# Kernel tuning notes

Hardware: AMD Instinct MI355X
Metric: run time of the kernel (lower is better)

## Reference

```python
import jax, jax.numpy as jnp
import numpy as np

B, L, S, E = 16, 2048, 2048, 512

def setup_inputs() -> dict:
    key = jax.random.key(0)
    k1, k2, k3 = jax.random.split(key, 3)
    queries = jax.random.normal(k1, (B, L, E), dtype=jnp.float32)
    keys = jax.random.normal(k2, (B, S, E), dtype=jnp.float32)
    values = jax.random.normal(k3, (B, S, E), dtype=jnp.float32)
    # default causal mask: True above the diagonal (positions to mask out)
    attn_mask = jnp.triu(jnp.ones((L, S), dtype=bool), k=1)
    return {"queries": queries, "keys": keys, "values": values, "attn_mask": attn_mask}

def reference(queries, keys, values, attn_mask):
    # queries [B,L,E], keys/values [B,S,E], attn_mask [L,S] bool (True = mask)
    scale = 1.0 / jnp.sqrt(jnp.asarray(queries.shape[-1], queries.dtype))
    scores = jnp.einsum('ble,bse->bls', queries, keys)  # [B,L,S]
    scores = jnp.where(attn_mask, -jnp.inf, scores) * scale
    attn = jax.nn.softmax(scores, axis=-1)  # dropout p=0.0 -> identity
    context = jnp.einsum('bls,bse->ble', attn, values)  # [B,L,E]
    return context
```

## Files before the change

### kernel.cpp

```cpp
#include <hip/hip_runtime.h>

typedef __attribute__((ext_vector_type(4))) float f32x4;
typedef __attribute__((ext_vector_type(16))) float f32x16;
typedef __attribute__((ext_vector_type(8))) short s16x8;
typedef __attribute__((ext_vector_type(8))) unsigned short u16x8;
typedef __attribute__((ext_vector_type(4))) unsigned short u16x4;

#define NB 16
#define SEQ 2048
#define DIM 512
#define QB 64
#define KB 512

__device__ __forceinline__ unsigned short f2bf(float x) {
  unsigned u = __float_as_uint(x);
  u += 0x7fffu + ((u >> 16) & 1u);
  return (unsigned short)(u >> 16);
}

__global__ __launch_bounds__(256) void kf_cvt_kernel(const float* __restrict__ in,
                                                     unsigned short* __restrict__ out) {
  __shared__ float ld[32 * 513];
  const float cs = 0.0637587224f;
  int blk = blockIdx.x;
  int b = blk >> 6, kv32 = blk & 63;
  int t = threadIdx.x;
  const float* src = in + ((size_t)b * SEQ + kv32 * 32) * DIM;
#pragma unroll
  for (int i = 0; i < 16; ++i) {
    int flat = (i * 256 + t) * 4;
    f32x4 a = *(const f32x4*)(src + flat);
    int row = flat >> 9, e = flat & 511;
    float* d = ld + row * 513 + e;
    d[0] = a[0]; d[1] = a[1]; d[2] = a[2]; d[3] = a[3];
  }
  __syncthreads();
  unsigned short* dst = out + (size_t)blk * 16384;
#pragma unroll
  for (int i = 0; i < 8; ++i) {
    int idx8 = i * 256 + t;
    int kstep = idx8 >> 6, ln = idx8 & 63;
    int row = ln & 31, hi = ln >> 5;
    const float* s = ld + row * 513 + kstep * 16 + hi * 8;
    u16x8 o;
#pragma unroll
    for (int j = 0; j < 8; ++j) o[j] = f2bf(s[j] * cs);
    *(u16x8*)(dst + (size_t)idx8 * 8) = o;
  }
}

__global__ __launch_bounds__(256) void vf_cvt_kernel(const float* __restrict__ in,
                                                     unsigned short* __restrict__ out) {
  __shared__ float ld[256 * 33];
  int blk = blockIdx.x;
  int kvc = blk & 7, e32 = (blk >> 3) & 15, b = blk >> 7;
  int t = threadIdx.x;
  const float* src = in + ((size_t)b * SEQ + kvc * 256) * DIM + e32 * 32;
  int r0 = t >> 2, part = t & 3;
#pragma unroll
  for (int i = 0; i < 4; ++i) {
    int row = i * 64 + r0;
    const float* s = src + (size_t)row * DIM + part * 8;
    f32x4 a0 = *(const f32x4*)s;
    f32x4 a1 = *(const f32x4*)(s + 4);
    float* d = ld + row * 33 + part * 8;
    d[0] = a0[0]; d[1] = a0[1]; d[2] = a0[2]; d[3] = a0[3];
    d[4] = a1[0]; d[5] = a1[1]; d[6] = a1[2]; d[7] = a1[3];
  }
  __syncthreads();
  unsigned short* dst = out + (size_t)blk * 8192;
#pragma unroll
  for (int i = 0; i < 4; ++i) {
    int idx8 = i * 256 + t;
    int ksl = idx8 >> 6, ln = idx8 & 63;
    int e = ln & 31, hi = ln >> 5;
    const float* s0 = ld + (ksl * 16 + hi * 8) * 33 + e;
    u16x8 o;
#pragma unroll
    for (int j = 0; j < 8; ++j) o[j] = f2bf(s0[j * 33]);
    *(u16x8*)(dst + (size_t)idx8 * 8) = o;
  }
}

__global__ __launch_bounds__(1024, 1) void attn_kernel(const float* __restrict__ qg,
                                                       const unsigned short* __restrict__ kf,
                                                       const unsigned short* __restrict__ vf,
                                                       float* __restrict__ out) {
  int b = blockIdx.x;
  int y = blockIdx.y;
  int qt = (y < 16) ? y : 47 - y;
  int q0 = qt * QB;

  int tid = threadIdx.x;
  int lane = tid & 63;
  int wid = tid >> 6;
  int l31 = lane & 31;
  int lhi = lane >> 5;
  int kvq = wid;

  __shared__ unsigned short Qs[2][32][512];
  __shared__ unsigned short Pl[64][512];
  __shared__ float cmxT[64][20];
  __shared__ float Fs[64];
  __shared__ float Ls[64];

  {
    int q = tid >> 4;
    int ec = (tid & 15) * 32;
    const float* src = qg + ((size_t)b * SEQ + q0 + q) * DIM + ec;
    float v[32];
#pragma unroll
    for (int i = 0; i < 8; ++i) {
      f32x4 a = *(const f32x4*)(src + i * 4);
      v[i * 4 + 0] = a[0]; v[i * 4 + 1] = a[1]; v[i * 4 + 2] = a[2]; v[i * 4 + 3] = a[3];
    }
    int mgq = q >> 5, lq = q & 31;
#pragma unroll
    for (int s = 0; s < 2; ++s) {
      int ks = (ec >> 4) + s;
#pragma unroll
      for (int h = 0; h < 2; ++h) {
        u16x8 o;
#pragma unroll
        for (int j = 0; j < 8; ++j) o[j] = f2bf(v[s * 16 + h * 8 + j]);
        *(u16x8*)&Qs[mgq][ks][(lq + 32 * h) * 8] = o;
      }
    }
  }
  __syncthreads();

  f32x16 oacc[2];
#pragma unroll
  for (int n = 0; n < 2; ++n)
#pragma unroll
    for (int r = 0; r < 16; ++r) oacc[n][r] = 0.f;

  float m0 = -1e30f, m1 = -1e30f, l0 = 0.f, l1 = 0.f;
  unsigned swz = ((unsigned)l31) << 5;

  const unsigned short* kfb = kf + ((size_t)b * 64) * 16384;
  const unsigned short* vfb = vf + ((size_t)b * 16 + wid) * 128 * 512;
  int nt = (qt + 8) >> 3;

  for (int t = 0; t < nt; ++t) {
    int kvb = t * 512 + kvq * 32;
    bool act = kvb <= q0 + 63;

    f32x16 s0, s1;
    if (act) {
#pragma unroll
      for (int r = 0; r < 16; ++r) { s0[r] = 0.f; s1[r] = 0.f; }
      const unsigned short* kp = kfb + ((size_t)(t * 16 + kvq) * 32) * 512 + lane * 8;
#pragma unroll 4
      for (int ks = 0; ks < 32; ++ks) {
        s16x8 a = *(const s16x8*)(kp + ks * 512);
        s16x8 b0 = *(const s16x8*)&Qs[0][ks][lane * 8];
        s16x8 b1 = *(const s16x8*)&Qs[1][ks][lane * 8];
        s0 = __builtin_amdgcn_mfma_f32_32x32x16_bf16(a, b0, s0, 0, 0, 0);
        s1 = __builtin_amdgcn_mfma_f32_32x32x16_bf16(a, b1, s1, 0, 0, 0);
      }
      if (t == nt - 1) {
#pragma unroll
        for (int r = 0; r < 16; ++r) {
          int kv = kvb + (r & 3) + 8 * (r >> 2) + 4 * lhi;
          if (kv > q0 + l31) s0[r] = -1e30f;
          if (kv > q0 + 32 + l31) s1[r] = -1e30f;
        }
      }
    } else {
#pragma unroll
      for (int r = 0; r < 16; ++r) { s0[r] = -1e30f; s1[r] = -1e30f; }
    }

    {
      float cm0 = s0[0], cm1 = s1[0];
#pragma unroll
      for (int r = 1; r < 16; ++r) { cm0 = fmaxf(cm0, s0[r]); cm1 = fmaxf(cm1, s1[r]); }
      cm0 = fmaxf(cm0, __shfl_xor(cm0, 32));
      cm1 = fmaxf(cm1, __shfl_xor(cm1, 32));
      if (lhi == 0) { cmxT[l31][kvq] = cm0; cmxT[32 + l31][kvq] = cm1; }
    }
    __syncthreads();

    float fsc0, fsc1;
    {
      f32x4 c0 = *(const f32x4*)&cmxT[l31][0];
      f32x4 c1 = *(const f32x4*)&cmxT[l31][4];
      f32x4 c2 = *(const f32x4*)&cmxT[l31][8];
      f32x4 c3 = *(const f32x4*)&cmxT[l31][12];
      float mt = fmaxf(fmaxf(fmaxf(c0[0], c0[1]), fmaxf(c0[2], c0[3])),
                       fmaxf(fmaxf(c1[0], c1[1]), fmaxf(c1[2], c1[3])));
      mt = fmaxf(mt, fmaxf(fmaxf(fmaxf(c2[0], c2[1]), fmaxf(c2[2], c2[3])),
                           fmaxf(fmaxf(c3[0], c3[1]), fmaxf(c3[2], c3[3]))));
      float mn = fmaxf(m0, mt);
      fsc0 = exp2f(m0 - mn);
      m0 = mn;
      float ps = 0.f;
      u16x4 pk[4];
#pragma unroll
      for (int r = 0; r < 16; ++r) {
        float p = exp2f(s0[r] - mn);
        ps += p;
        pk[r >> 2][r & 3] = f2bf(p);
      }
      l0 = l0 * fsc0 + ps;
      char* prow = (char*)&Pl[l31][0];
#pragma unroll
      for (int g = 0; g < 4; ++g) {
        unsigned kvbyte = (unsigned)(kvq * 64 + g * 16 + lhi * 8);
        *(u16x4*)(prow + (kvbyte ^ swz)) = pk[g];
      }
    }
    {
      f32x4 c0 = *(const f32x4*)&cmxT[32 + l31][0];
      f32x4 c1 = *(const f32x4*)&cmxT[32 + l31][4];
      f32x4 c2 = *(const f32x4*)&cmxT[32 + l31][8];
      f32x4 c3 = *(const f32x4*)&cmxT[32 + l31][12];
      float mt = fmaxf(fmaxf(fmaxf(c0[0], c0[1]), fmaxf(c0[2], c0[3])),
                       fmaxf(fmaxf(c1[0], c1[1]), fmaxf(c1[2], c1[3])));
      mt = fmaxf(mt, fmaxf(fmaxf(fmaxf(c2[0], c2[1]), fmaxf(c2[2], c2[3])),
                           fmaxf(fmaxf(c3[0], c3[1]), fmaxf(c3[2], c3[3]))));
      float mn = fmaxf(m1, mt);
      fsc1 = exp2f(m1 - mn);
      m1 = mn;
      float ps = 0.f;
      u16x4 pk[4];
#pragma unroll
      for (int r = 0; r < 16; ++r) {
        float p = exp2f(s1[r] - mn);
        ps += p;
        pk[r >> 2][r & 3] = f2bf(p);
      }
      l1 = l1 * fsc1 + ps;
      char* prow = (char*)&Pl[32 + l31][0];
#pragma unroll
      for (int g = 0; g < 4; ++g) {
        unsigned kvbyte = (unsigned)(kvq * 64 + g * 16 + lhi * 8);
        *(u16x4*)(prow + (kvbyte ^ swz)) = pk[g];
      }
    }
    if (wid == 0 && lhi == 0) { Fs[l31] = fsc0; Fs[32 + l31] = fsc1; }
    __syncthreads();

    {
      f32x4 fr[2][4];
#pragma unroll
      for (int m2 = 0; m2 < 2; ++m2)
#pragma unroll
        for (int g = 0; g < 4; ++g)
          fr[m2][g] = *(const f32x4*)&Fs[m2 * 32 + g * 8 + lhi * 4];
#pragma unroll
      for (int m2 = 0; m2 < 2; ++m2)
#pragma unroll
        for (int r = 0; r < 16; ++r) oacc[m2][r] *= fr[m2][r >> 2][r & 3];

      int kvcnt = q0 + 64 - t * 512;
      if (kvcnt > 512) kvcnt = 512;
      int ksb = (kvcnt + 15) >> 4;
      const unsigned short* vp = vfb + (size_t)(t * 32) * 512 + lane * 8;
      const char* pr0 = (const char*)&Pl[l31][0];
      const char* pr1 = (const char*)&Pl[32 + l31][0];
#pragma unroll 4
      for (int ks = 0; ks < ksb; ++ks) {
        unsigned kb0 = (unsigned)(ks * 32 + lhi * 16);
        s16x8 A0 = *(const s16x8*)(pr0 + (kb0 ^ swz));
        s16x8 A1 = *(const s16x8*)(pr1 + (kb0 ^ swz));
        s16x8 B0 = *(const s16x8*)(vp + ks * 512);
        oacc[0] = __builtin_amdgcn_mfma_f32_32x32x16_bf16(A0, B0, oacc[0], 0, 0, 0);
        oacc[1] = __builtin_amdgcn_mfma_f32_32x32x16_bf16(A1, B0, oacc[1], 0, 0, 0);
      }
    }
  }

  {
    float* lsx = (float*)&Qs[0][0][0];
    lsx[(kvq * 2 + lhi) * 68 + l31] = l0;
    lsx[(kvq * 2 + lhi) * 68 + 32 + l31] = l1;
    __syncthreads();
    if (tid < 64) {
      float s = 0.f;
#pragma unroll
      for (int c = 0; c < 32; ++c) s += lsx[c * 68 + tid];
      Ls[tid] = 1.f / s;
    }
    __syncthreads();
  }

  {
    f32x4 li[2][4];
#pragma unroll
    for (int m2 = 0; m2 < 2; ++m2)
#pragma unroll
      for (int g = 0; g < 4; ++g)
        li[m2][g] = *(const f32x4*)&Ls[m2 * 32 + g * 8 + lhi * 4];
#pragma unroll
    for (int m2 = 0; m2 < 2; ++m2)
#pragma unroll
      for (int r = 0; r < 16; ++r) {
        int row = m2 * 32 + (r & 3) + 8 * (r >> 2) + 4 * lhi;
        out[((size_t)b * SEQ + q0 + row) * DIM + wid * 32 + l31] =
            oacc[m2][r] * li[m2][r >> 2][r & 3];
      }
  }
}

extern "C" void kernel_launch(void* const* d_in, const int* in_sizes, int n_in,
                              void* d_out, int out_size, void* d_ws, size_t ws_size,
                              hipStream_t stream) {
  (void)in_sizes; (void)n_in; (void)out_size;
  const float* q = (const float*)d_in[0];
  const float* k = (const float*)d_in[1];
  const float* v = (const float*)d_in[2];
  float* out = (float*)d_out;
  const size_t nelem = (size_t)NB * SEQ * DIM;
  if (ws_size < 2 * nelem * sizeof(unsigned short)) return;
  unsigned short* kfw = (unsigned short*)d_ws;
  unsigned short* vfw = kfw + nelem;

  kf_cvt_kernel<<<NB * 64, 256, 0, stream>>>(k, kfw);
  vf_cvt_kernel<<<NB * 16 * 8, 256, 0, stream>>>(v, vfw);
  dim3 ag(NB, SEQ / QB);
  attn_kernel<<<ag, 1024, 0, stream>>>(q, kfw, vfw, out);
}
```

Baseline: 154.9 us.

## Remap attention grid per XCD, relax occupancy bounds, change P swizzle

Replaces the 2D grid with a 1D grid of 512 blocks. Batch is chosen from the XCD index so blocks that share K/V land on the same XCD's L2, and query tiles are issued longest-first. Swaps launch_bounds(1024,1) for amdgpu_waves_per_eu(4,4), changes the Pl LDS swizzle to an 8-row, 16-byte XOR pattern, and raises the QK loop unroll to 8. The aim is better L2 locality, load balance and fewer LDS bank conflicts, at the risk of register-pressure changes and a causal-work imbalance across XCDs.

```diff
diff --git a/kernel.cpp b/kernel.cpp
--- a/kernel.cpp
+++ b/kernel.cpp
@@ -82,13 +82,17 @@
   }
 }
 
-__global__ __launch_bounds__(1024, 1) void attn_kernel(const float* __restrict__ qg,
-                                                       const unsigned short* __restrict__ kf,
-                                                       const unsigned short* __restrict__ vf,
-                                                       float* __restrict__ out) {
-  int b = blockIdx.x;
-  int y = blockIdx.y;
-  int qt = (y < 16) ? y : 47 - y;
+__global__ __launch_bounds__(1024)
+__attribute__((amdgpu_waves_per_eu(4, 4)))
+void attn_kernel(const float* __restrict__ qg,
+                 const unsigned short* __restrict__ kf,
+                 const unsigned short* __restrict__ vf,
+                 float* __restrict__ out) {
+  int id = blockIdx.x;
+  int xcd = id & 7;
+  int s = id >> 3;
+  int b = xcd + ((s >= 32) ? 8 : 0);
+  int qt = 31 - (s & 31);
   int q0 = qt * QB;
 
   int tid = threadIdx.x;
@@ -116,13 +120,13 @@
     }
     int mgq = q >> 5, lq = q & 31;
 #pragma unroll
-    for (int s = 0; s < 2; ++s) {
-      int ks = (ec >> 4) + s;
+    for (int ss = 0; ss < 2; ++ss) {
+      int ks = (ec >> 4) + ss;
 #pragma unroll
       for (int h = 0; h < 2; ++h) {
         u16x8 o;
 #pragma unroll
-        for (int j = 0; j < 8; ++j) o[j] = f2bf(v[s * 16 + h * 8 + j]);
+        for (int j = 0; j < 8; ++j) o[j] = f2bf(v[ss * 16 + h * 8 + j]);
         *(u16x8*)&Qs[mgq][ks][(lq + 32 * h) * 8] = o;
       }
     }
@@ -136,7 +140,7 @@
     for (int r = 0; r < 16; ++r) oacc[n][r] = 0.f;
 
   float m0 = -1e30f, m1 = -1e30f, l0 = 0.f, l1 = 0.f;
-  unsigned swz = ((unsigned)l31) << 5;
+  unsigned swz = ((unsigned)(l31 & 7)) << 4;
 
   const unsigned short* kfb = kf + ((size_t)b * 64) * 16384;
   const unsigned short* vfb = vf + ((size_t)b * 16 + wid) * 128 * 512;
@@ -151,7 +155,7 @@
 #pragma unroll
       for (int r = 0; r < 16; ++r) { s0[r] = 0.f; s1[r] = 0.f; }
       const unsigned short* kp = kfb + ((size_t)(t * 16 + kvq) * 32) * 512 + lane * 8;
-#pragma unroll 4
+#pragma unroll 8
       for (int ks = 0; ks < 32; ++ks) {
         s16x8 a = *(const s16x8*)(kp + ks * 512);
         s16x8 b0 = *(const s16x8*)&Qs[0][ks][lane * 8];
@@ -182,7 +186,6 @@
     }
     __syncthreads();
 
-    float fsc0, fsc1;
     {
       f32x4 c0 = *(const f32x4*)&cmxT[l31][0];
       f32x4 c1 = *(const f32x4*)&cmxT[l31][4];
@@ -193,7 +196,7 @@
       mt = fmaxf(mt, fmaxf(fmaxf(fmaxf(c2[0], c2[1]), fmaxf(c2[2], c2[3])),
                            fmaxf(fmaxf(c3[0], c3[1]), fmaxf(c3[2], c3[3]))));
       float mn = fmaxf(m0, mt);
-      fsc0 = exp2f(m0 - mn);
+      float fsc0 = exp2f(m0 - mn);
       m0 = mn;
       float ps = 0.f;
       u16x4 pk[4];
@@ -210,6 +213,7 @@
         unsigned kvbyte = (unsigned)(kvq * 64 + g * 16 + lhi * 8);
         *(u16x4*)(prow + (kvbyte ^ swz)) = pk[g];
       }
+      if (wid == 0 && lhi == 0) Fs[l31] = fsc0;
     }
     {
       f32x4 c0 = *(const f32x4*)&cmxT[32 + l31][0];
@@ -221,7 +225,7 @@
       mt = fmaxf(mt, fmaxf(fmaxf(fmaxf(c2[0], c2[1]), fmaxf(c2[2], c2[3])),
                            fmaxf(fmaxf(c3[0], c3[1]), fmaxf(c3[2], c3[3]))));
       float mn = fmaxf(m1, mt);
-      fsc1 = exp2f(m1 - mn);
+      float fsc1 = exp2f(m1 - mn);
       m1 = mn;
       float ps = 0.f;
       u16x4 pk[4];
@@ -238,8 +242,8 @@
         unsigned kvbyte = (unsigned)(kvq * 64 + g * 16 + lhi * 8);
         *(u16x4*)(prow + (kvbyte ^ swz)) = pk[g];
       }
-    }
-    if (wid == 0 && lhi == 0) { Fs[l31] = fsc0; Fs[32 + l31] = fsc1; }
+      if (wid == 0 && lhi == 0) Fs[32 + l31] = fsc1;
+    }
     __syncthreads();
 
     {
@@ -278,10 +282,10 @@
     lsx[(kvq * 2 + lhi) * 68 + 32 + l31] = l1;
     __syncthreads();
     if (tid < 64) {
-      float s = 0.f;
-#pragma unroll
-      for (int c = 0; c < 32; ++c) s += lsx[c * 68 + tid];
-      Ls[tid] = 1.f / s;
+      float sum = 0.f;
+#pragma unroll
+      for (int c = 0; c < 32; ++c) sum += lsx[c * 68 + tid];
+      Ls[tid] = 1.f / sum;
     }
     __syncthreads();
   }
@@ -319,6 +323,5 @@
 
   kf_cvt_kernel<<<NB * 64, 256, 0, stream>>>(k, kfw);
   vf_cvt_kernel<<<NB * 16 * 8, 256, 0, stream>>>(v, vfw);
-  dim3 ag(NB, SEQ / QB);
-  attn_kernel<<<ag, 1024, 0, stream>>>(q, kfw, vfw, out);
-}
+  attn_kernel<<<512, 1024, 0, stream>>>(q, kfw, vfw, out);
+}
```

Result: no change. 156.7 us (+1.2%).
